# Kernel optimization log

Measured on AMD Instinct MI355X. Metric: run time of the kernel, lower is better.

## Reference

```python
import jax, jax.numpy as jnp
from jax import lax
import numpy as np

HID = 1000


def _lstm_cell(x, h, c, W_ih, W_hh, b_ih, b_hh):
    # PyTorch nn.LSTMCell gate order: i, f, g, o
    gates = x @ W_ih.T + b_ih + h @ W_hh.T + b_hh  # [B, 4H]
    i, f, g, o = jnp.split(gates, 4, axis=-1)
    c2 = jax.nn.sigmoid(f) * c + jax.nn.sigmoid(i) * jnp.tanh(g)
    h2 = jax.nn.sigmoid(o) * jnp.tanh(c2)
    return h2, c2


def setup_inputs() -> dict:
    key = jax.random.key(0)
    ks = jax.random.split(key, 8)
    B, T, nbones = 256, 49, 64
    D = nbones * 3
    s = 0.05
    inp = {"enc_in": jax.random.normal(ks[0], (B, T, D), jnp.float32)}
    dims = [D, HID, HID]
    for l in range(3):
        inp[f"W_ih{l}"] = jax.random.normal(ks[1 + 2 * l], (4 * HID, dims[l]), jnp.float32) * s
        inp[f"W_hh{l}"] = jax.random.normal(ks[2 + 2 * l], (4 * HID, HID), jnp.float32) * s
        inp[f"b_ih{l}"] = jnp.zeros((4 * HID,), jnp.float32)
        inp[f"b_hh{l}"] = jnp.zeros((4 * HID,), jnp.float32)
    inp["train"] = 0  # eval mode: dropout is identity
    return inp


def reference(enc_in, W_ih0, W_hh0, b_ih0, b_hh0,
              W_ih1, W_hh1, b_ih1, b_hh1,
              W_ih2, W_hh2, b_ih2, b_hh2, train):
    params = [(W_ih0, W_hh0, b_ih0, b_hh0),
              (W_ih1, W_hh1, b_ih1, b_hh1),
              (W_ih2, W_hh2, b_ih2, b_hh2)]
    B = enc_in.shape[0]
    zeros = jnp.zeros((B, HID), enc_in.dtype)
    init = (tuple(zeros for _ in range(3)), tuple(zeros for _ in range(3)))

    def step(carry, x):
        hs, cs = carry
        new_h, new_c = [], []
        inp = x
        for l in range(3):
            h2, c2 = _lstm_cell(inp, hs[l], cs[l], *params[l])
            new_h.append(h2)
            new_c.append(c2)
            inp = h2  # dropout with train=False is identity
        return (tuple(new_h), tuple(new_c)), jnp.stack(new_h)  # [3, B, H]

    # scan over time: enc_in [B, T, D] -> [T, B, D]
    _, ys = lax.scan(step, init, jnp.transpose(enc_in, (1, 0, 2)))
    # ys: [T, 3, B, H] -> [3, B, T, H]; equals the original per-layer `output`
    out = jnp.transpose(ys, (1, 2, 0, 3))
    return out
```

## Files before the change

kernel.cpp:

```cpp
#include <hip/hip_runtime.h>

#define HID_ 1000
#define NB 256
#define TT 49
#define DIN 192
#define NPAD 1024
#define M_ALL (TT * NB)

typedef _Float16 f16;
typedef _Float16 f16x8 __attribute__((ext_vector_type(8)));
typedef float f32x4 __attribute__((ext_vector_type(4)));
typedef const __attribute__((address_space(1))) unsigned int* gas_u32;
typedef __attribute__((address_space(3))) unsigned int* las_u32;

__device__ __forceinline__ float sigmf_(float x) {
    return 1.0f / (1.0f + __expf(-x));
}
__device__ __forceinline__ float tanhf_(float x) {
    float ax = fabsf(x);
    float e = __expf(-2.0f * ax);
    float t = (1.0f - e) / (1.0f + e);
    return copysignf(t, x);
}

__global__ void conv_weight(const float* __restrict__ src, f16* __restrict__ dst,
                            int K, int KPADv) {
    size_t total = 4ull * NPAD * KPADv;
    for (size_t idx = (size_t)blockIdx.x * blockDim.x + threadIdx.x; idx < total;
         idx += (size_t)gridDim.x * blockDim.x) {
        int kp = (int)(idx % KPADv);
        size_t rest = idx / KPADv;
        int np = (int)(rest % NPAD);
        int g = (int)(rest / NPAD);
        f16 v = (f16)0.0f;
        if (np < HID_ && kp < K) v = (f16)src[(size_t)(g * HID_ + np) * K + kp];
        dst[idx] = v;
    }
}

__global__ void conv_x(const float* __restrict__ src, f16* __restrict__ dst) {
    size_t total = (size_t)TT * NB * DIN;
    for (size_t idx = (size_t)blockIdx.x * blockDim.x + threadIdx.x; idx < total;
         idx += (size_t)gridDim.x * blockDim.x) {
        int k = (int)(idx % DIN);
        size_t rest = idx / DIN;
        int b = (int)(rest % NB);
        int t = (int)(rest / NB);
        dst[idx] = (f16)src[((size_t)b * TT + t) * DIN + k];
    }
}

__global__ void conv_bias(const float* __restrict__ bih, const float* __restrict__ bhh,
                          float* __restrict__ dst) {
    int idx = blockIdx.x * blockDim.x + threadIdx.x;
    if (idx < 4 * NPAD) {
        int np = idx & (NPAD - 1);
        int g = idx >> 10;
        float v = 0.0f;
        if (np < HID_) v = bih[g * HID_ + np] + bhh[g * HID_ + np];
        dst[idx] = v;
    }
}

__global__ __launch_bounds__(256) void input_gemm(
    const f16* __restrict__ A, int lda, int kiters,
    const f16* __restrict__ W, int ldw,
    const float* __restrict__ bias,
    f16* __restrict__ pre2) {
    __shared__ f16 As[128 * 64];
    __shared__ f16 Bs[128 * 64];
    const int id = blockIdx.x;
    const int sw = (id & 7) * (gridDim.x >> 3) + (id >> 3);
    const int m0 = (sw >> 5) << 7;
    const int n0 = (sw & 31) << 7;
    const int w = threadIdx.x >> 6;
    const int lane = threadIdx.x & 63;
    const int r = lane & 15;
    const int kb8 = (lane >> 4) << 3;
    const int wm = (w >> 1) << 6, wn = (w & 1) << 6;
    const int strow = (w << 5) + (lane >> 3);
    const int stcol = (lane & 7) << 3;

    f32x4 acc[4][4];
#pragma unroll
    for (int i = 0; i < 4; i++)
#pragma unroll
        for (int j = 0; j < 4; j++) acc[i][j] = (f32x4){0.f, 0.f, 0.f, 0.f};

    for (int kt = 0; kt < kiters; kt++) {
        const int k0 = kt << 6;
#pragma unroll
        for (int q = 0; q < 4; q++) {
            const int row = strow + (q << 3);
            const int cbase = ((w << 5) + (q << 3)) << 6;
            const f16* ga = A + (size_t)(m0 + row) * lda + k0 + stcol;
            const f16* gb = W + (size_t)(n0 + row) * ldw + k0 + stcol;
            __builtin_amdgcn_global_load_lds((gas_u32)ga, (las_u32)(As + cbase), 16, 0, 0);
            __builtin_amdgcn_global_load_lds((gas_u32)gb, (las_u32)(Bs + cbase), 16, 0, 0);
        }
        __syncthreads();
#pragma unroll
        for (int ks = 0; ks < 2; ks++) {
            f16x8 av[4], bv[4];
#pragma unroll
            for (int i = 0; i < 4; i++)
                av[i] = *(const f16x8*)(As + ((wm + i * 16 + r) << 6) + (ks << 5) + kb8);
#pragma unroll
            for (int j = 0; j < 4; j++)
                bv[j] = *(const f16x8*)(Bs + ((wn + j * 16 + r) << 6) + (ks << 5) + kb8);
#pragma unroll
            for (int i = 0; i < 4; i++)
#pragma unroll
                for (int j = 0; j < 4; j++)
                    acc[i][j] = __builtin_amdgcn_mfma_f32_16x16x32_f16(av[i], bv[j], acc[i][j], 0, 0, 0);
        }
        __syncthreads();
    }

    const int rbase = (lane >> 4) << 2;
#pragma unroll
    for (int j = 0; j < 4; j++) {
        const int gcol = n0 + wn + j * 16 + r;
        const float bj = bias[gcol];
        const int g = gcol >> 10, cl = gcol & 1023;
        const int jt2 = cl >> 5, c = cl & 31;
        const int n2 = c >> 4, r2 = c & 15;
#pragma unroll
        for (int i = 0; i < 4; i++) {
#pragma unroll
            for (int q = 0; q < 4; q++) {
                const int grow = m0 + wm + i * 16 + rbase + q;
                const int t_ = grow >> 8, b = grow & 255;
                const int bt2 = b >> 5, lb = b & 31;
                const int mi = lb >> 4, u2 = (lb >> 2) & 3, q2 = lb & 3;
                const int l2 = u2 * 16 + r2, flat = mi * 8 + n2 * 4 + q2;
                pre2[((((size_t)t_ * 8 + bt2) * 32 + jt2) * 4 + g) * 1024 + l2 * 16 + flat] =
                    (f16)(acc[i][j][q] + bj);
            }
        }
    }
}

__global__ __launch_bounds__(512, 2) void rec_persist(
    const f16* __restrict__ Whh, const f16* __restrict__ pre2,
    f16* __restrict__ hall, float* __restrict__ outl,
    unsigned int* __restrict__ flags) {
    __shared__ __align__(16) char smem[64 * 1024];
    float* pl = (float*)smem;
    const int bid = blockIdx.x;
    const int bt = bid & 7;
    const int jt = bid >> 3;
    const int b0 = bt << 5;
    const int jc0 = jt << 5;
    const int tid = threadIdx.x;
    const int w = tid >> 6;
    const int g = w >> 1;
    const int kh = w & 1;
    const int lane = tid & 63;
    const int r = lane & 15;
    const int u = lane >> 4;
    const int kbb = u << 4;
    const int rbase = u << 2;
    const int swz = (r & 7) << 4;

    f16x8 wreg[2][16];
#pragma unroll
    for (int n = 0; n < 2; n++) {
        const f16* wp = Whh + ((size_t)(g * NPAD + jc0 + n * 16 + r)) * NPAD + (kh << 9) + (u << 3);
#pragma unroll
        for (int ks = 0; ks < 16; ks++) wreg[n][ks] = *(const f16x8*)(wp + ks * 32);
    }

    const int eb = tid >> 4;
    const int ej = (tid & 15) << 1;
    float cv[2] = {0.f, 0.f};
    unsigned int* myflags = flags + bt * TT;
    const size_t preblk = ((((size_t)bt) * 32 + jt) * 4 + g) * 1024 + lane * 16;

    auto LOADP = [&](int tindex, f16x8& pa, f16x8& pb) {
        if (kh == 0) {
            const f16* pp = pre2 + (size_t)tindex * 8 * 32 * 4 * 1024 + preblk;
            pa = *(const f16x8*)pp;
            pb = *(const f16x8*)(pp + 8);
        }
    };

    auto STEP = [&](int t, f16x8& pc0, f16x8& pc1, f16x8& pn0, f16x8& pn1) {
        if (t > 0) {
            if (tid == 0) {
                while (__hip_atomic_load(myflags + (t - 1), __ATOMIC_RELAXED,
                                         __HIP_MEMORY_SCOPE_AGENT) < 32u) {}
            }
            __syncthreads();
            asm volatile("" ::: "memory");
            const f16* hread = hall + (size_t)(t - 1) * NB * NPAD;
#pragma unroll
            for (int i = 0; i < 8; i++) {
                int c = tid + (i << 9);
                int row = c >> 7;
                int cb = (c & 127) << 4;
                f16x8 v = *(const f16x8*)(hread + (size_t)(b0 + row) * NPAD + (cb >> 1));
                *(f16x8*)(smem + row * 2048 + (cb ^ ((row & 7) << 4))) = v;
            }
            __syncthreads();
        }

        LOADP(t + 1 < TT ? t + 1 : t, pn0, pn1);

        f32x4 acc[2][2];
#pragma unroll
        for (int mi = 0; mi < 2; mi++)
#pragma unroll
            for (int n = 0; n < 2; n++)
#pragma unroll
                for (int q = 0; q < 4; q++) {
                    if (kh == 0)
                        acc[mi][n][q] = (float)(mi == 0 ? pc0[n * 4 + q] : pc1[n * 4 + q]);
                    else
                        acc[mi][n][q] = 0.f;
                }

        if (t > 0) {
#pragma unroll
            for (int ks = 0; ks < 16; ks++) {
                const int ksg = (kh << 4) + ks;
                f16x8 a0 = *(const f16x8*)(smem + r * 2048 + ((ksg * 64 + kbb) ^ swz));
                f16x8 a1 = *(const f16x8*)(smem + (16 + r) * 2048 + ((ksg * 64 + kbb) ^ swz));
                acc[0][0] = __builtin_amdgcn_mfma_f32_16x16x32_f16(a0, wreg[0][ks], acc[0][0], 0, 0, 0);
                acc[0][1] = __builtin_amdgcn_mfma_f32_16x16x32_f16(a0, wreg[1][ks], acc[0][1], 0, 0, 0);
                acc[1][0] = __builtin_amdgcn_mfma_f32_16x16x32_f16(a1, wreg[0][ks], acc[1][0], 0, 0, 0);
                acc[1][1] = __builtin_amdgcn_mfma_f32_16x16x32_f16(a1, wreg[1][ks], acc[1][1], 0, 0, 0);
            }
        }
        __syncthreads();

        if (kh == 1) {
#pragma unroll
            for (int mi = 0; mi < 2; mi++)
#pragma unroll
                for (int n = 0; n < 2; n++)
#pragma unroll
                    for (int q = 0; q < 4; q++)
                        pl[(g * 32 + mi * 16 + rbase + q) * 36 + n * 16 + r] = acc[mi][n][q];
        }
        __syncthreads();
        if (kh == 0) {
#pragma unroll
            for (int mi = 0; mi < 2; mi++)
#pragma unroll
                for (int n = 0; n < 2; n++)
#pragma unroll
                    for (int q = 0; q < 4; q++) {
                        const int idx = (g * 32 + mi * 16 + rbase + q) * 36 + n * 16 + r;
                        pl[idx] = pl[idx] + acc[mi][n][q];
                    }
        }
        __syncthreads();

        float hvv[2];
#pragma unroll
        for (int q = 0; q < 2; q++) {
            float i_ = pl[(0 * 32 + eb) * 36 + ej + q];
            float f_ = pl[(1 * 32 + eb) * 36 + ej + q];
            float g_ = pl[(2 * 32 + eb) * 36 + ej + q];
            float o_ = pl[(3 * 32 + eb) * 36 + ej + q];
            float cn = sigmf_(f_) * cv[q] + sigmf_(i_) * tanhf_(g_);
            hvv[q] = sigmf_(o_) * tanhf_(cn);
            cv[q] = cn;
        }
        {
            union { f16 h2[2]; unsigned uu; } cvt;
            cvt.h2[0] = (f16)hvv[0];
            cvt.h2[1] = (f16)hvv[1];
            __hip_atomic_store(
                (unsigned*)(hall + ((size_t)t * NB + b0 + eb) * NPAD + jc0 + ej), cvt.uu,
                __ATOMIC_RELAXED, __HIP_MEMORY_SCOPE_AGENT);
        }
        const int col = jc0 + ej;
        if (col < HID_) {
            *(float2*)(outl + ((size_t)(b0 + eb) * TT + t) * HID_ + col) =
                make_float2(hvv[0], hvv[1]);
        }
        __syncthreads();
        if (tid == 0)
            __hip_atomic_fetch_add(myflags + t, 1u, __ATOMIC_RELAXED, __HIP_MEMORY_SCOPE_AGENT);
    };

    f16x8 pA0 = {}, pA1 = {}, pB0 = {}, pB1 = {};
    LOADP(0, pA0, pA1);
    for (int t = 0; t < TT; t += 2) {
        STEP(t, pA0, pA1, pB0, pB1);
        if (t + 1 < TT) STEP(t + 1, pB0, pB1, pA0, pA1);
    }
}

extern "C" void kernel_launch(void* const* d_in, const int* in_sizes, int n_in,
                              void* d_out, int out_size, void* d_ws, size_t ws_size,
                              hipStream_t stream) {
    const float* enc_in = (const float*)d_in[0];
    const float* W_ih[3] = {(const float*)d_in[1], (const float*)d_in[5], (const float*)d_in[9]};
    const float* W_hh[3] = {(const float*)d_in[2], (const float*)d_in[6], (const float*)d_in[10]};
    const float* b_ih[3] = {(const float*)d_in[3], (const float*)d_in[7], (const float*)d_in[11]};
    const float* b_hh[3] = {(const float*)d_in[4], (const float*)d_in[8], (const float*)d_in[12]};
    float* out = (float*)d_out;

    char* ws = (char*)d_ws;
    size_t off = 0;
    auto alloc = [&](size_t bytes) {
        char* p = ws + off;
        off += (bytes + 255) & ~(size_t)255;
        return p;
    };
    f16* Wih_c[3];
    f16* Whh_c[3];
    Wih_c[0] = (f16*)alloc(4ull * NPAD * DIN * sizeof(f16));
    Whh_c[0] = (f16*)alloc(4ull * NPAD * NPAD * sizeof(f16));
    Wih_c[1] = (f16*)alloc(4ull * NPAD * NPAD * sizeof(f16));
    Whh_c[1] = (f16*)alloc(4ull * NPAD * NPAD * sizeof(f16));
    Wih_c[2] = (f16*)alloc(4ull * NPAD * NPAD * sizeof(f16));
    Whh_c[2] = (f16*)alloc(4ull * NPAD * NPAD * sizeof(f16));
    float* bias_c[3];
    for (int l = 0; l < 3; l++) bias_c[l] = (float*)alloc(4ull * NPAD * sizeof(float));
    f16* xbf = (f16*)alloc((size_t)TT * NB * DIN * sizeof(f16));
    f16* hall[3];
    for (int l = 0; l < 3; l++) hall[l] = (f16*)alloc((size_t)TT * NB * NPAD * sizeof(f16));
    f16* pre2 = (f16*)alloc((size_t)M_ALL * 4096 * sizeof(f16));
    unsigned int* flags = (unsigned int*)alloc(3ull * 8 * TT * sizeof(unsigned int));

    hipMemsetAsync(flags, 0, 3ull * 8 * TT * sizeof(unsigned int), stream);

    conv_weight<<<512, 256, 0, stream>>>(W_ih[0], Wih_c[0], DIN, DIN);
    conv_weight<<<2048, 256, 0, stream>>>(W_hh[0], Whh_c[0], HID_, NPAD);
    conv_weight<<<2048, 256, 0, stream>>>(W_ih[1], Wih_c[1], HID_, NPAD);
    conv_weight<<<2048, 256, 0, stream>>>(W_hh[1], Whh_c[1], HID_, NPAD);
    conv_weight<<<2048, 256, 0, stream>>>(W_ih[2], Wih_c[2], HID_, NPAD);
    conv_weight<<<2048, 256, 0, stream>>>(W_hh[2], Whh_c[2], HID_, NPAD);
    conv_x<<<1024, 256, 0, stream>>>(enc_in, xbf);
    for (int l = 0; l < 3; l++)
        conv_bias<<<(4 * NPAD + 255) / 256, 256, 0, stream>>>(b_ih[l], b_hh[l], bias_c[l]);

    for (int l = 0; l < 3; l++) {
        if (l == 0)
            input_gemm<<<3136, 256, 0, stream>>>(xbf, DIN, DIN / 64, Wih_c[0], DIN,
                                                 bias_c[0], pre2);
        else
            input_gemm<<<3136, 256, 0, stream>>>(hall[l - 1], NPAD, NPAD / 64, Wih_c[l], NPAD,
                                                 bias_c[l], pre2);
        rec_persist<<<256, 512, 0, stream>>>(
            Whh_c[l], pre2, hall[l], out + (size_t)l * NB * TT * HID_,
            flags + (size_t)l * 8 * TT);
    }
}
```

Before: 1.157 ms.

## Overlap h staging with MFMA in recurrent kernel and vectorize pre-activation stores

```diff
diff --git a/kernel.cpp b/kernel.cpp
--- a/kernel.cpp
+++ b/kernel.cpp
@@ -5,9 +5,10 @@
 #define TT 49
 #define DIN 192
 #define NPAD 1024
-#define M_ALL (TT * NB)
+#define M_ALL (TT * 256)
 
 typedef _Float16 f16;
+typedef _Float16 f16x4 __attribute__((ext_vector_type(4)));
 typedef _Float16 f16x8 __attribute__((ext_vector_type(8)));
 typedef float f32x4 __attribute__((ext_vector_type(4)));
 typedef const __attribute__((address_space(1))) unsigned int* gas_u32;
@@ -76,7 +77,8 @@
     const int w = threadIdx.x >> 6;
     const int lane = threadIdx.x & 63;
     const int r = lane & 15;
-    const int kb8 = (lane >> 4) << 3;
+    const int u = lane >> 4;
+    const int kb8 = u << 3;
     const int wm = (w >> 1) << 6, wn = (w & 1) << 6;
     const int strow = (w << 5) + (lane >> 3);
     const int stcol = (lane & 7) << 3;
@@ -117,7 +119,6 @@
         __syncthreads();
     }
 
-    const int rbase = (lane >> 4) << 2;
 #pragma unroll
     for (int j = 0; j < 4; j++) {
         const int gcol = n0 + wn + j * 16 + r;
@@ -125,18 +126,18 @@
         const int g = gcol >> 10, cl = gcol & 1023;
         const int jt2 = cl >> 5, c = cl & 31;
         const int n2 = c >> 4, r2 = c & 15;
+        const int l2 = u * 16 + r2;
 #pragma unroll
         for (int i = 0; i < 4; i++) {
-#pragma unroll
-            for (int q = 0; q < 4; q++) {
-                const int grow = m0 + wm + i * 16 + rbase + q;
-                const int t_ = grow >> 8, b = grow & 255;
-                const int bt2 = b >> 5, lb = b & 31;
-                const int mi = lb >> 4, u2 = (lb >> 2) & 3, q2 = lb & 3;
-                const int l2 = u2 * 16 + r2, flat = mi * 8 + n2 * 4 + q2;
-                pre2[((((size_t)t_ * 8 + bt2) * 32 + jt2) * 4 + g) * 1024 + l2 * 16 + flat] =
-                    (f16)(acc[i][j][q] + bj);
-            }
+            const int grow = m0 + wm + i * 16 + (u << 2);
+            const int t_ = grow >> 8, b = grow & 255;
+            const int bt2 = b >> 5;
+            const int mi = i & 1;
+            f16x4 hv;
+#pragma unroll
+            for (int q = 0; q < 4; q++) hv[q] = (f16)(acc[i][j][q] + bj);
+            *(f16x4*)(pre2 + ((((size_t)t_ * 8 + bt2) * 32 + jt2) * 4 + g) * 1024 +
+                      l2 * 16 + mi * 8 + n2 * 4) = hv;
         }
     }
 }
@@ -146,7 +147,7 @@
     f16* __restrict__ hall, float* __restrict__ outl,
     unsigned int* __restrict__ flags) {
     __shared__ __align__(16) char smem[64 * 1024];
-    float* pl = (float*)smem;
+    __shared__ float pl[4 * 32 * 36];
     const int bid = blockIdx.x;
     const int bt = bid & 7;
     const int jt = bid >> 3;
@@ -176,6 +177,7 @@
     float cv[2] = {0.f, 0.f};
     unsigned int* myflags = flags + bt * TT;
     const size_t preblk = ((((size_t)bt) * 32 + jt) * 4 + g) * 1024 + lane * 16;
+    const int tau = ((w >> 1) << 6) + lane;
 
     auto LOADP = [&](int tindex, f16x8& pa, f16x8& pb) {
         if (kh == 0) {
@@ -186,26 +188,25 @@
     };
 
     auto STEP = [&](int t, f16x8& pc0, f16x8& pc1, f16x8& pn0, f16x8& pn1) {
+        LOADP(t + 1 < TT ? t + 1 : t, pn0, pn1);
+
+        const f16* hread = hall + (size_t)(t - 1) * NB * NPAD;
         if (t > 0) {
-            if (tid == 0) {
-                while (__hip_atomic_load(myflags + (t - 1), __ATOMIC_RELAXED,
-                                         __HIP_MEMORY_SCOPE_AGENT) < 32u) {}
+            while (__hip_atomic_load(myflags + (t - 1), __ATOMIC_RELAXED,
+                                     __HIP_MEMORY_SCOPE_AGENT) < 32u) {}
+            asm volatile("" ::: "memory");
+            if (kh == 1) {
+#pragma unroll
+                for (int i2 = 0; i2 < 8; i2++) {
+                    int c = tau + (i2 << 8);
+                    int row = c >> 6;
+                    int boff = (c & 63) << 4;
+                    f16x8 v = *(const f16x8*)(hread + (size_t)(b0 + row) * NPAD + (boff >> 1));
+                    *(f16x8*)(smem + row * 2048 + (boff ^ ((row & 7) << 4))) = v;
+                }
             }
-            __syncthreads();
-            asm volatile("" ::: "memory");
-            const f16* hread = hall + (size_t)(t - 1) * NB * NPAD;
-#pragma unroll
-            for (int i = 0; i < 8; i++) {
-                int c = tid + (i << 9);
-                int row = c >> 7;
-                int cb = (c & 127) << 4;
-                f16x8 v = *(const f16x8*)(hread + (size_t)(b0 + row) * NPAD + (cb >> 1));
-                *(f16x8*)(smem + row * 2048 + (cb ^ ((row & 7) << 4))) = v;
-            }
-            __syncthreads();
-        }
-
-        LOADP(t + 1 < TT ? t + 1 : t, pn0, pn1);
+        }
+        __syncthreads();
 
         f32x4 acc[2][2];
 #pragma unroll
@@ -220,7 +221,7 @@
                         acc[mi][n][q] = 0.f;
                 }
 
-        if (t > 0) {
+        auto MFMA16 = [&]() {
 #pragma unroll
             for (int ks = 0; ks < 16; ks++) {
                 const int ksg = (kh << 4) + ks;
@@ -231,10 +232,26 @@
                 acc[1][0] = __builtin_amdgcn_mfma_f32_16x16x32_f16(a1, wreg[0][ks], acc[1][0], 0, 0, 0);
                 acc[1][1] = __builtin_amdgcn_mfma_f32_16x16x32_f16(a1, wreg[1][ks], acc[1][1], 0, 0, 0);
             }
-        }
-        __syncthreads();
-
-        if (kh == 1) {
+        };
+
+        if (t > 0) {
+            if (kh == 0) {
+                MFMA16();
+            } else {
+#pragma unroll
+                for (int i2 = 0; i2 < 8; i2++) {
+                    int c = tau + (i2 << 8);
+                    int row = c >> 6;
+                    int boff = 1024 + ((c & 63) << 4);
+                    f16x8 v = *(const f16x8*)(hread + (size_t)(b0 + row) * NPAD + (boff >> 1));
+                    *(f16x8*)(smem + row * 2048 + (boff ^ ((row & 7) << 4))) = v;
+                }
+            }
+        }
+        __syncthreads();
+
+        if (t > 0 && kh == 1) MFMA16();
+        if (kh == 0) {
 #pragma unroll
             for (int mi = 0; mi < 2; mi++)
 #pragma unroll
@@ -244,7 +261,8 @@
                         pl[(g * 32 + mi * 16 + rbase + q) * 36 + n * 16 + r] = acc[mi][n][q];
         }
         __syncthreads();
-        if (kh == 0) {
+
+        if (t > 0 && kh == 1) {
 #pragma unroll
             for (int mi = 0; mi < 2; mi++)
 #pragma unroll
@@ -260,10 +278,11 @@
         float hvv[2];
 #pragma unroll
         for (int q = 0; q < 2; q++) {
-            float i_ = pl[(0 * 32 + eb) * 36 + ej + q];
-            float f_ = pl[(1 * 32 + eb) * 36 + ej + q];
-            float g_ = pl[(2 * 32 + eb) * 36 + ej + q];
-            float o_ = pl[(3 * 32 + eb) * 36 + ej + q];
+            const int c0 = ej + q;
+            float i_ = pl[(0 * 32 + eb) * 36 + c0];
+            float f_ = pl[(1 * 32 + eb) * 36 + c0];
+            float g_ = pl[(2 * 32 + eb) * 36 + c0];
+            float o_ = pl[(3 * 32 + eb) * 36 + c0];
             float cn = sigmf_(f_) * cv[q] + sigmf_(i_) * tanhf_(g_);
             hvv[q] = sigmf_(o_) * tanhf_(cn);
             cv[q] = cn;
@@ -276,14 +295,14 @@
                 (unsigned*)(hall + ((size_t)t * NB + b0 + eb) * NPAD + jc0 + ej), cvt.uu,
                 __ATOMIC_RELAXED, __HIP_MEMORY_SCOPE_AGENT);
         }
+        __syncthreads();
+        if (tid == 0)
+            __hip_atomic_fetch_add(myflags + t, 1u, __ATOMIC_RELAXED, __HIP_MEMORY_SCOPE_AGENT);
         const int col = jc0 + ej;
         if (col < HID_) {
             *(float2*)(outl + ((size_t)(b0 + eb) * TT + t) * HID_ + col) =
                 make_float2(hvv[0], hvv[1]);
         }
-        __syncthreads();
-        if (tid == 0)
-            __hip_atomic_fetch_add(myflags + t, 1u, __ATOMIC_RELAXED, __HIP_MEMORY_SCOPE_AGENT);
     };
 
     f16x8 pA0 = {}, pA1 = {}, pB0 = {}, pB1 = {};
```

After: 1.511 ms. +30.5%, slower.

## Split recurrent K across four waves, async LDS h-load, reorder flag signal

Applied to the files above, without the earlier changes.

```diff
diff --git a/kernel.cpp b/kernel.cpp
--- a/kernel.cpp
+++ b/kernel.cpp
@@ -5,9 +5,10 @@
 #define TT 49
 #define DIN 192
 #define NPAD 1024
-#define M_ALL (TT * NB)
+#define M_ALL (TT * 256)
 
 typedef _Float16 f16;
+typedef _Float16 f16x4 __attribute__((ext_vector_type(4)));
 typedef _Float16 f16x8 __attribute__((ext_vector_type(8)));
 typedef float f32x4 __attribute__((ext_vector_type(4)));
 typedef const __attribute__((address_space(1))) unsigned int* gas_u32;
@@ -76,7 +77,8 @@
     const int w = threadIdx.x >> 6;
     const int lane = threadIdx.x & 63;
     const int r = lane & 15;
-    const int kb8 = (lane >> 4) << 3;
+    const int u = lane >> 4;
+    const int kb8 = u << 3;
     const int wm = (w >> 1) << 6, wn = (w & 1) << 6;
     const int strow = (w << 5) + (lane >> 3);
     const int stcol = (lane & 7) << 3;
@@ -117,26 +119,26 @@
         __syncthreads();
     }
 
-    const int rbase = (lane >> 4) << 2;
 #pragma unroll
     for (int j = 0; j < 4; j++) {
         const int gcol = n0 + wn + j * 16 + r;
         const float bj = bias[gcol];
-        const int g = gcol >> 10, cl = gcol & 1023;
-        const int jt2 = cl >> 5, c = cl & 31;
-        const int n2 = c >> 4, r2 = c & 15;
+        const int g = gcol >> 10;
+        const int cl = gcol & 1023;
+        const int jt2 = cl >> 5;
+        const int n2 = (cl >> 4) & 1;
 #pragma unroll
         for (int i = 0; i < 4; i++) {
-#pragma unroll
-            for (int q = 0; q < 4; q++) {
-                const int grow = m0 + wm + i * 16 + rbase + q;
-                const int t_ = grow >> 8, b = grow & 255;
-                const int bt2 = b >> 5, lb = b & 31;
-                const int mi = lb >> 4, u2 = (lb >> 2) & 3, q2 = lb & 3;
-                const int l2 = u2 * 16 + r2, flat = mi * 8 + n2 * 4 + q2;
-                pre2[((((size_t)t_ * 8 + bt2) * 32 + jt2) * 4 + g) * 1024 + l2 * 16 + flat] =
-                    (f16)(acc[i][j][q] + bj);
-            }
+            const int grow = m0 + wm + i * 16 + (u << 2);
+            const int t_ = grow >> 8;
+            const int bt2 = (grow >> 5) & 7;
+            const int mi = i & 1;
+            f16x4 hv;
+#pragma unroll
+            for (int q = 0; q < 4; q++) hv[q] = (f16)(acc[i][j][q] + bj);
+            const int slot = (u << 4) + r;
+            *(f16x4*)(pre2 + (((size_t)t_ * 8 + bt2) * 32 + jt2) * 4096 +
+                      (size_t)slot * 64 + g * 16 + n2 * 8 + mi * 4) = hv;
         }
     }
 }
@@ -146,7 +148,7 @@
     f16* __restrict__ hall, float* __restrict__ outl,
     unsigned int* __restrict__ flags) {
     __shared__ __align__(16) char smem[64 * 1024];
-    float* pl = (float*)smem;
+    __shared__ float pl[4 * 4 * 32 * 34];
     const int bid = blockIdx.x;
     const int bt = bid & 7;
     const int jt = bid >> 3;
@@ -154,118 +156,116 @@
     const int jc0 = jt << 5;
     const int tid = threadIdx.x;
     const int w = tid >> 6;
-    const int g = w >> 1;
-    const int kh = w & 1;
+    const int gp = w >> 2;
+    const int kh = w & 3;
     const int lane = tid & 63;
     const int r = lane & 15;
     const int u = lane >> 4;
-    const int kbb = u << 4;
-    const int rbase = u << 2;
     const int swz = (r & 7) << 4;
 
-    f16x8 wreg[2][16];
-#pragma unroll
-    for (int n = 0; n < 2; n++) {
-        const f16* wp = Whh + ((size_t)(g * NPAD + jc0 + n * 16 + r)) * NPAD + (kh << 9) + (u << 3);
-#pragma unroll
-        for (int ks = 0; ks < 16; ks++) wreg[n][ks] = *(const f16x8*)(wp + ks * 32);
-    }
+    f16x8 wreg[2][2][8];
+#pragma unroll
+    for (int gl = 0; gl < 2; gl++)
+#pragma unroll
+        for (int n = 0; n < 2; n++) {
+            const f16* wp = Whh + ((size_t)((2 * gp + gl) * NPAD + jc0 + n * 16 + r)) * NPAD +
+                            (kh << 8) + (u << 3);
+#pragma unroll
+            for (int ks = 0; ks < 8; ks++) wreg[gl][n][ks] = *(const f16x8*)(wp + ks * 32);
+        }
 
     const int eb = tid >> 4;
     const int ej = (tid & 15) << 1;
     float cv[2] = {0.f, 0.f};
     unsigned int* myflags = flags + bt * TT;
-    const size_t preblk = ((((size_t)bt) * 32 + jt) * 4 + g) * 1024 + lane * 16;
-
-    auto LOADP = [&](int tindex, f16x8& pa, f16x8& pb) {
+    const size_t preblk = (((size_t)bt * 32 + jt) * 4096) + (size_t)lane * 64 + gp * 32;
+
+    auto LOADP = [&](int tindex, f16x8 (&pc)[4]) {
         if (kh == 0) {
-            const f16* pp = pre2 + (size_t)tindex * 8 * 32 * 4 * 1024 + preblk;
-            pa = *(const f16x8*)pp;
-            pb = *(const f16x8*)(pp + 8);
+            const f16* pp = pre2 + (size_t)tindex * 8 * 32 * 4096 + preblk;
+#pragma unroll
+            for (int c = 0; c < 4; c++) pc[c] = *(const f16x8*)(pp + c * 8);
         }
     };
 
-    auto STEP = [&](int t, f16x8& pc0, f16x8& pc1, f16x8& pn0, f16x8& pn1) {
+    auto STEP = [&](int t, f16x8 (&pc)[4], f16x8 (&pn)[4]) {
+        LOADP(t + 1 < TT ? t + 1 : t, pn);
+
         if (t > 0) {
-            if (tid == 0) {
-                while (__hip_atomic_load(myflags + (t - 1), __ATOMIC_RELAXED,
-                                         __HIP_MEMORY_SCOPE_AGENT) < 32u) {}
+            while (__hip_atomic_load(myflags + (t - 1), __ATOMIC_RELAXED,
+                                     __HIP_MEMORY_SCOPE_AGENT) < 32u) {}
+            asm volatile("" ::: "memory");
+            const char* hread = (const char*)(hall + (size_t)(t - 1) * NB * NPAD);
+#pragma unroll
+            for (int i = 0; i < 8; i++) {
+                const int c = tid + (i << 9);
+                const int row = c >> 7;
+                const int cb = (c & 127) << 4;
+                const char* gsrc = hread + ((size_t)(b0 + row) << 11) + (cb ^ ((row & 7) << 4));
+                __builtin_amdgcn_global_load_lds((gas_u32)gsrc,
+                                                 (las_u32)(smem + (w << 10) + (i << 13)), 16, 0, 0);
             }
-            __syncthreads();
-            asm volatile("" ::: "memory");
-            const f16* hread = hall + (size_t)(t - 1) * NB * NPAD;
-#pragma unroll
-            for (int i = 0; i < 8; i++) {
-                int c = tid + (i << 9);
-                int row = c >> 7;
-                int cb = (c & 127) << 4;
-                f16x8 v = *(const f16x8*)(hread + (size_t)(b0 + row) * NPAD + (cb >> 1));
-                *(f16x8*)(smem + row * 2048 + (cb ^ ((row & 7) << 4))) = v;
+        }
+        __syncthreads();
+
+        f32x4 acc[2][2][2];
+#pragma unroll
+        for (int mi = 0; mi < 2; mi++)
+#pragma unroll
+            for (int gl = 0; gl < 2; gl++)
+#pragma unroll
+                for (int n = 0; n < 2; n++)
+#pragma unroll
+                    for (int q = 0; q < 4; q++)
+                        acc[mi][gl][n][q] = (kh == 0) ? (float)pc[gl * 2 + n][mi * 4 + q] : 0.f;
+
+        if (t > 0) {
+#pragma unroll
+            for (int ks = 0; ks < 8; ks++) {
+                const int kb = ((kh * 8 + ks) << 6) + (u << 4);
+                f16x8 a0 = *(const f16x8*)(smem + r * 2048 + (kb ^ swz));
+                f16x8 a1 = *(const f16x8*)(smem + (16 + r) * 2048 + (kb ^ swz));
+#pragma unroll
+                for (int gl = 0; gl < 2; gl++)
+#pragma unroll
+                    for (int n = 0; n < 2; n++) {
+                        acc[0][gl][n] = __builtin_amdgcn_mfma_f32_16x16x32_f16(
+                            a0, wreg[gl][n][ks], acc[0][gl][n], 0, 0, 0);
+                        acc[1][gl][n] = __builtin_amdgcn_mfma_f32_16x16x32_f16(
+                            a1, wreg[gl][n][ks], acc[1][gl][n], 0, 0, 0);
+                    }
             }
-            __syncthreads();
-        }
-
-        LOADP(t + 1 < TT ? t + 1 : t, pn0, pn1);
-
-        f32x4 acc[2][2];
+        }
 #pragma unroll
         for (int mi = 0; mi < 2; mi++)
 #pragma unroll
-            for (int n = 0; n < 2; n++)
-#pragma unroll
-                for (int q = 0; q < 4; q++) {
-                    if (kh == 0)
-                        acc[mi][n][q] = (float)(mi == 0 ? pc0[n * 4 + q] : pc1[n * 4 + q]);
-                    else
-                        acc[mi][n][q] = 0.f;
-                }
-
-        if (t > 0) {
-#pragma unroll
-            for (int ks = 0; ks < 16; ks++) {
-                const int ksg = (kh << 4) + ks;
-                f16x8 a0 = *(const f16x8*)(smem + r * 2048 + ((ksg * 64 + kbb) ^ swz));
-                f16x8 a1 = *(const f16x8*)(smem + (16 + r) * 2048 + ((ksg * 64 + kbb) ^ swz));
-                acc[0][0] = __builtin_amdgcn_mfma_f32_16x16x32_f16(a0, wreg[0][ks], acc[0][0], 0, 0, 0);
-                acc[0][1] = __builtin_amdgcn_mfma_f32_16x16x32_f16(a0, wreg[1][ks], acc[0][1], 0, 0, 0);
-                acc[1][0] = __builtin_amdgcn_mfma_f32_16x16x32_f16(a1, wreg[0][ks], acc[1][0], 0, 0, 0);
-                acc[1][1] = __builtin_amdgcn_mfma_f32_16x16x32_f16(a1, wreg[1][ks], acc[1][1], 0, 0, 0);
+            for (int gl = 0; gl < 2; gl++)
+#pragma unroll
+                for (int n = 0; n < 2; n++)
+#pragma unroll
+                    for (int q = 0; q < 4; q++)
+                        pl[((kh * 4 + 2 * gp + gl) * 32 + mi * 16 + u * 4 + q) * 34 +
+                           n * 16 + r] = acc[mi][gl][n][q];
+        __syncthreads();
+
+        float gv[4][2];
+#pragma unroll
+        for (int gate = 0; gate < 4; gate++) {
+            float2 s = make_float2(0.f, 0.f);
+#pragma unroll
+            for (int k2 = 0; k2 < 4; k2++) {
+                float2 p = *(const float2*)&pl[((k2 * 4 + gate) * 32 + eb) * 34 + ej];
+                s.x += p.x;
+                s.y += p.y;
             }
-        }
-        __syncthreads();
-
-        if (kh == 1) {
-#pragma unroll
-            for (int mi = 0; mi < 2; mi++)
-#pragma unroll
-                for (int n = 0; n < 2; n++)
-#pragma unroll
-                    for (int q = 0; q < 4; q++)
-                        pl[(g * 32 + mi * 16 + rbase + q) * 36 + n * 16 + r] = acc[mi][n][q];
-        }
-        __syncthreads();
-        if (kh == 0) {
-#pragma unroll
-            for (int mi = 0; mi < 2; mi++)
-#pragma unroll
-                for (int n = 0; n < 2; n++)
-#pragma unroll
-                    for (int q = 0; q < 4; q++) {
-                        const int idx = (g * 32 + mi * 16 + rbase + q) * 36 + n * 16 + r;
-                        pl[idx] = pl[idx] + acc[mi][n][q];
-                    }
-        }
-        __syncthreads();
-
+            gv[gate][0] = s.x;
+            gv[gate][1] = s.y;
+        }
         float hvv[2];
 #pragma unroll
         for (int q = 0; q < 2; q++) {
-            float i_ = pl[(0 * 32 + eb) * 36 + ej + q];
-            float f_ = pl[(1 * 32 + eb) * 36 + ej + q];
-            float g_ = pl[(2 * 32 + eb) * 36 + ej + q];
-            float o_ = pl[(3 * 32 + eb) * 36 + ej + q];
-            float cn = sigmf_(f_) * cv[q] + sigmf_(i_) * tanhf_(g_);
-            hvv[q] = sigmf_(o_) * tanhf_(cn);
+            float cn = sigmf_(gv[1][q]) * cv[q] + sigmf_(gv[0][q]) * tanhf_(gv[2][q]);
+            hvv[q] = sigmf_(gv[3][q]) * tanhf_(cn);
             cv[q] = cn;
         }
         {
@@ -276,21 +276,21 @@
                 (unsigned*)(hall + ((size_t)t * NB + b0 + eb) * NPAD + jc0 + ej), cvt.uu,
                 __ATOMIC_RELAXED, __HIP_MEMORY_SCOPE_AGENT);
         }
+        __syncthreads();
+        if (tid == 0)
+            __hip_atomic_fetch_add(myflags + t, 1u, __ATOMIC_RELAXED, __HIP_MEMORY_SCOPE_AGENT);
         const int col = jc0 + ej;
         if (col < HID_) {
             *(float2*)(outl + ((size_t)(b0 + eb) * TT + t) * HID_ + col) =
                 make_float2(hvv[0], hvv[1]);
         }
-        __syncthreads();
-        if (tid == 0)
-            __hip_atomic_fetch_add(myflags + t, 1u, __ATOMIC_RELAXED, __HIP_MEMORY_SCOPE_AGENT);
     };
 
-    f16x8 pA0 = {}, pA1 = {}, pB0 = {}, pB1 = {};
-    LOADP(0, pA0, pA1);
+    f16x8 pA[4] = {}, pB[4] = {};
+    LOADP(0, pA);
     for (int t = 0; t < TT; t += 2) {
-        STEP(t, pA0, pA1, pB0, pB1);
-        if (t + 1 < TT) STEP(t + 1, pB0, pB1, pA0, pA1);
+        STEP(t, pA, pB);
+        if (t + 1 < TT) STEP(t + 1, pB, pA);
     }
 }
 
```

New measurement: 1.268 ms. 1.1x slower.

## Trim barriers in recurrent step and vectorize pre-activation stores

Applied to the files above, without the earlier changes.

```diff
diff --git a/kernel.cpp b/kernel.cpp
--- a/kernel.cpp
+++ b/kernel.cpp
@@ -5,9 +5,10 @@
 #define TT 49
 #define DIN 192
 #define NPAD 1024
-#define M_ALL (TT * NB)
+#define M_ALL (TT * 256)
 
 typedef _Float16 f16;
+typedef _Float16 f16x4 __attribute__((ext_vector_type(4)));
 typedef _Float16 f16x8 __attribute__((ext_vector_type(8)));
 typedef float f32x4 __attribute__((ext_vector_type(4)));
 typedef const __attribute__((address_space(1))) unsigned int* gas_u32;
@@ -76,7 +77,8 @@
     const int w = threadIdx.x >> 6;
     const int lane = threadIdx.x & 63;
     const int r = lane & 15;
-    const int kb8 = (lane >> 4) << 3;
+    const int u = lane >> 4;
+    const int kb8 = u << 3;
     const int wm = (w >> 1) << 6, wn = (w & 1) << 6;
     const int strow = (w << 5) + (lane >> 3);
     const int stcol = (lane & 7) << 3;
@@ -117,7 +119,6 @@
         __syncthreads();
     }
 
-    const int rbase = (lane >> 4) << 2;
 #pragma unroll
     for (int j = 0; j < 4; j++) {
         const int gcol = n0 + wn + j * 16 + r;
@@ -125,18 +126,18 @@
         const int g = gcol >> 10, cl = gcol & 1023;
         const int jt2 = cl >> 5, c = cl & 31;
         const int n2 = c >> 4, r2 = c & 15;
+        const int l2 = u * 16 + r2;
 #pragma unroll
         for (int i = 0; i < 4; i++) {
-#pragma unroll
-            for (int q = 0; q < 4; q++) {
-                const int grow = m0 + wm + i * 16 + rbase + q;
-                const int t_ = grow >> 8, b = grow & 255;
-                const int bt2 = b >> 5, lb = b & 31;
-                const int mi = lb >> 4, u2 = (lb >> 2) & 3, q2 = lb & 3;
-                const int l2 = u2 * 16 + r2, flat = mi * 8 + n2 * 4 + q2;
-                pre2[((((size_t)t_ * 8 + bt2) * 32 + jt2) * 4 + g) * 1024 + l2 * 16 + flat] =
-                    (f16)(acc[i][j][q] + bj);
-            }
+            const int grow = m0 + wm + i * 16 + (u << 2);
+            const int t_ = grow >> 8;
+            const int bt2 = (grow >> 5) & 7;
+            const int mi = i & 1;
+            f16x4 hv;
+#pragma unroll
+            for (int q = 0; q < 4; q++) hv[q] = (f16)(acc[i][j][q] + bj);
+            *(f16x4*)(pre2 + ((((size_t)t_ * 8 + bt2) * 32 + jt2) * 4 + g) * 1024 +
+                      l2 * 16 + mi * 8 + n2 * 4) = hv;
         }
     }
 }
@@ -146,7 +147,7 @@
     f16* __restrict__ hall, float* __restrict__ outl,
     unsigned int* __restrict__ flags) {
     __shared__ __align__(16) char smem[64 * 1024];
-    float* pl = (float*)smem;
+    __shared__ float pl[2 * 4 * 32 * 34];
     const int bid = blockIdx.x;
     const int bt = bid & 7;
     const int jt = bid >> 3;
@@ -186,12 +187,11 @@
     };
 
     auto STEP = [&](int t, f16x8& pc0, f16x8& pc1, f16x8& pn0, f16x8& pn1) {
+        LOADP(t + 1 < TT ? t + 1 : t, pn0, pn1);
+
         if (t > 0) {
-            if (tid == 0) {
-                while (__hip_atomic_load(myflags + (t - 1), __ATOMIC_RELAXED,
-                                         __HIP_MEMORY_SCOPE_AGENT) < 32u) {}
-            }
-            __syncthreads();
+            while (__hip_atomic_load(myflags + (t - 1), __ATOMIC_RELAXED,
+                                     __HIP_MEMORY_SCOPE_AGENT) < 32u) {}
             asm volatile("" ::: "memory");
             const f16* hread = hall + (size_t)(t - 1) * NB * NPAD;
 #pragma unroll
@@ -202,10 +202,8 @@
                 f16x8 v = *(const f16x8*)(hread + (size_t)(b0 + row) * NPAD + (cb >> 1));
                 *(f16x8*)(smem + row * 2048 + (cb ^ ((row & 7) << 4))) = v;
             }
-            __syncthreads();
-        }
-
-        LOADP(t + 1 < TT ? t + 1 : t, pn0, pn1);
+        }
+        __syncthreads();
 
         f32x4 acc[2][2];
 #pragma unroll
@@ -232,41 +230,33 @@
                 acc[1][1] = __builtin_amdgcn_mfma_f32_16x16x32_f16(a1, wreg[1][ks], acc[1][1], 0, 0, 0);
             }
         }
-        __syncthreads();
-
-        if (kh == 1) {
-#pragma unroll
-            for (int mi = 0; mi < 2; mi++)
-#pragma unroll
-                for (int n = 0; n < 2; n++)
-#pragma unroll
-                    for (int q = 0; q < 4; q++)
-                        pl[(g * 32 + mi * 16 + rbase + q) * 36 + n * 16 + r] = acc[mi][n][q];
-        }
-        __syncthreads();
-        if (kh == 0) {
-#pragma unroll
-            for (int mi = 0; mi < 2; mi++)
-#pragma unroll
-                for (int n = 0; n < 2; n++)
-#pragma unroll
-                    for (int q = 0; q < 4; q++) {
-                        const int idx = (g * 32 + mi * 16 + rbase + q) * 36 + n * 16 + r;
-                        pl[idx] = pl[idx] + acc[mi][n][q];
-                    }
-        }
+
+#pragma unroll
+        for (int mi = 0; mi < 2; mi++)
+#pragma unroll
+            for (int n = 0; n < 2; n++)
+#pragma unroll
+                for (int q = 0; q < 4; q++)
+                    pl[((kh * 4 + g) * 32 + mi * 16 + rbase + q) * 34 + n * 16 + r] =
+                        acc[mi][n][q];
         __syncthreads();
 
         float hvv[2];
-#pragma unroll
-        for (int q = 0; q < 2; q++) {
-            float i_ = pl[(0 * 32 + eb) * 36 + ej + q];
-            float f_ = pl[(1 * 32 + eb) * 36 + ej + q];
-            float g_ = pl[(2 * 32 + eb) * 36 + ej + q];
-            float o_ = pl[(3 * 32 + eb) * 36 + ej + q];
-            float cn = sigmf_(f_) * cv[q] + sigmf_(i_) * tanhf_(g_);
-            hvv[q] = sigmf_(o_) * tanhf_(cn);
-            cv[q] = cn;
+        {
+            float gv[4][2];
+#pragma unroll
+            for (int gate = 0; gate < 4; gate++) {
+                float2 p0 = *(const float2*)&pl[((0 * 4 + gate) * 32 + eb) * 34 + ej];
+                float2 p1 = *(const float2*)&pl[((1 * 4 + gate) * 32 + eb) * 34 + ej];
+                gv[gate][0] = p0.x + p1.x;
+                gv[gate][1] = p0.y + p1.y;
+            }
+#pragma unroll
+            for (int q = 0; q < 2; q++) {
+                float cn = sigmf_(gv[1][q]) * cv[q] + sigmf_(gv[0][q]) * tanhf_(gv[2][q]);
+                hvv[q] = sigmf_(gv[3][q]) * tanhf_(cn);
+                cv[q] = cn;
+            }
         }
         {
             union { f16 h2[2]; unsigned uu; } cvt;
@@ -276,14 +266,14 @@
                 (unsigned*)(hall + ((size_t)t * NB + b0 + eb) * NPAD + jc0 + ej), cvt.uu,
                 __ATOMIC_RELAXED, __HIP_MEMORY_SCOPE_AGENT);
         }
+        __syncthreads();
+        if (tid == 0)
+            __hip_atomic_fetch_add(myflags + t, 1u, __ATOMIC_RELAXED, __HIP_MEMORY_SCOPE_AGENT);
         const int col = jc0 + ej;
         if (col < HID_) {
             *(float2*)(outl + ((size_t)(b0 + eb) * TT + t) * HID_ + col) =
                 make_float2(hvv[0], hvv[1]);
         }
-        __syncthreads();
-        if (tid == 0)
-            __hip_atomic_fetch_add(myflags + t, 1u, __ATOMIC_RELAXED, __HIP_MEMORY_SCOPE_AGENT);
     };
 
     f16x8 pA0 = {}, pA1 = {}, pB0 = {}, pB1 = {};
```

New measurement: 1.122 ms. -3.1%, faster.
